# Performance work log

Hardware: AMD Instinct MI355X
Metric: run time of the kernel (lower is better)

Reference implementation:

```python
import jax, jax.numpy as jnp
import numpy as np

B, N, DIM = 2, 2048, 2048
H, KVH, HD = 16, 4, 128
N_REP = H // KVH
SCALE = np.float32(HD ** -0.5)


def setup_inputs() -> dict:
    key = jax.random.key(0)
    ks = jax.random.split(key, 5)
    x = jax.random.normal(ks[0], (B, N, DIM), dtype=jnp.float32)
    mask = jnp.tril(jnp.ones((N, N), dtype=jnp.int32))[None, None]  # [1,1,N,N] causal
    Wq = jax.random.normal(ks[1], (DIM, H * HD), dtype=jnp.float32) * (DIM ** -0.5)
    Wk = jax.random.normal(ks[2], (DIM, KVH * HD), dtype=jnp.float32) * (DIM ** -0.5)
    Wv = jax.random.normal(ks[3], (DIM, KVH * HD), dtype=jnp.float32) * (DIM ** -0.5)
    Wo = jax.random.normal(ks[4], (H * HD, DIM), dtype=jnp.float32) * ((H * HD) ** -0.5)
    return {"x": x, "mask": mask, "Wq": Wq, "Wk": Wk, "Wv": Wv, "Wo": Wo}


def reference(x, mask, Wq, Wk, Wv, Wo):
    Bx, Nx, _ = x.shape
    # projections -> [B, heads, N, head_dim]
    q = (x @ Wq).reshape(Bx, Nx, H, HD).transpose(0, 2, 1, 3)
    k = (x @ Wk).reshape(Bx, Nx, KVH, HD).transpose(0, 2, 1, 3)
    v = (x @ Wv).reshape(Bx, Nx, KVH, HD).transpose(0, 2, 1, 3)
    # repeat_interleave KV heads to match query heads (GQA)
    k = jnp.repeat(k, N_REP, axis=1)
    v = jnp.repeat(v, N_REP, axis=1)
    attn = jnp.einsum('bhqd,bhkd->bhqk', q, k) * SCALE
    attn = jnp.where(mask == 0, jnp.float32(-jnp.inf), attn)
    attn = jax.nn.softmax(attn, axis=-1)
    out = jnp.einsum('bhqk,bhkd->bhqd', attn, v)
    out = out.transpose(0, 2, 1, 3).reshape(Bx, Nx, H * HD)
    return out @ Wo
```

## Files before the change

### kernel.cpp

```cpp
#include <hip/hip_runtime.h>
#include <hip/hip_bf16.h>
#include <math.h>

typedef __bf16 bf16;
typedef bf16 bf16x8 __attribute__((ext_vector_type(8)));
typedef bf16 bf16x4v __attribute__((ext_vector_type(4)));
typedef float f32x4 __attribute__((ext_vector_type(4)));

#define GLD16(g, l) __builtin_amdgcn_global_load_lds(                          \
    (__attribute__((address_space(1))) void*)(g),                              \
    (__attribute__((address_space(3))) void*)(l), 16, 0, 0)

#define MFMA16(a, b, c) __builtin_amdgcn_mfma_f32_16x16x32_bf16((a), (b), (c), 0, 0, 0)

#if __has_builtin(__builtin_amdgcn_exp2f)
#define EXP2F(x) __builtin_amdgcn_exp2f(x)
#else
#define EXP2F(x) exp2f(x)
#endif

__device__ __forceinline__ f32x4 shfl_xor4(f32x4 a, int m) {
  f32x4 r;
  #pragma unroll
  for (int i = 0; i < 4; i++) r[i] = __shfl_xor(a[i], m);
  return r;
}

__global__ void cast_f32_bf16(const float* __restrict__ in, bf16* __restrict__ out, int n4) {
  int i = blockIdx.x * blockDim.x + threadIdx.x;
  if (i < n4) {
    float4 v = ((const float4*)in)[i];
    bf16x4v o;
    o.x = (bf16)v.x; o.y = (bf16)v.y; o.z = (bf16)v.z; o.w = (bf16)v.w;
    ((bf16x4v*)out)[i] = o;
  }
}

__global__ void transpose_cast(const float* __restrict__ in, bf16* __restrict__ out,
                               int colsIn, int outStride, int outRowOff, float scale) {
  __shared__ float t[32][33];
  int c0 = blockIdx.x * 32, r0 = blockIdx.y * 32;
  int tx = threadIdx.x, ty = threadIdx.y;
  #pragma unroll
  for (int i = 0; i < 32; i += 8)
    t[ty + i][tx] = in[(size_t)(r0 + ty + i) * colsIn + (c0 + tx)];
  __syncthreads();
  #pragma unroll
  for (int i = 0; i < 32; i += 8)
    out[(size_t)(outRowOff + c0 + ty + i) * outStride + (r0 + tx)] = (bf16)(t[tx][ty + i] * scale);
}

__global__ void transpose_v(const bf16* __restrict__ QKV, bf16* __restrict__ Vg) {
  __shared__ bf16 t[32][34];
  int n0 = blockIdx.x * 32, d0 = blockIdx.y * 32;
  int bk = blockIdx.z;
  int b = bk >> 2, kvh = bk & 3;
  const bf16* src = QKV + (size_t)b * 2048 * 3072 + 2560 + kvh * 128;
  bf16* dst = Vg + (size_t)bk * 128 * 2048;
  int tx = threadIdx.x, ty = threadIdx.y;
  #pragma unroll
  for (int i = 0; i < 32; i += 8)
    t[ty + i][tx] = src[(size_t)(n0 + ty + i) * 3072 + (d0 + tx)];
  __syncthreads();
  #pragma unroll
  for (int i = 0; i < 32; i += 8)
    dst[(size_t)(d0 + ty + i) * 2048 + (n0 + tx)] = t[tx][ty + i];
}

template <typename OutT>
__global__ __launch_bounds__(256, 2) void gemm_bt(const bf16* __restrict__ A,
                                                  const bf16* __restrict__ Bt,
                                                  OutT* __restrict__ C,
                                                  int M, int N, int K) {
  __shared__ __attribute__((aligned(16))) bf16 As[128 * 32];
  __shared__ __attribute__((aligned(16))) bf16 Bs[128 * 32];
  const int tid = threadIdx.x;
  const int lane = tid & 63;
  const int wave = tid >> 6;
  const int wm = wave >> 1, wn = wave & 1;
  const int l15 = lane & 15, quad = lane >> 4;
  const int rowBase = blockIdx.y * 128;
  const int colBase = blockIdx.x * 128;

  f32x4 acc[4][4] = {};

  const int cb0 = wave * 64;
  const int c0 = cb0 + lane;
  const int c1 = c0 + 256;
  const bf16* a0 = A + (size_t)(rowBase + (c0 >> 2)) * K + (c0 & 3) * 8;
  const bf16* a1 = A + (size_t)(rowBase + (c1 >> 2)) * K + (c1 & 3) * 8;
  const bf16* b0 = Bt + (size_t)(colBase + (c0 >> 2)) * K + (c0 & 3) * 8;
  const bf16* b1 = Bt + (size_t)(colBase + (c1 >> 2)) * K + (c1 & 3) * 8;
  bf16* lA0 = &As[cb0 * 8];
  bf16* lA1 = &As[(cb0 + 256) * 8];
  bf16* lB0 = &Bs[cb0 * 8];
  bf16* lB1 = &Bs[(cb0 + 256) * 8];

  for (int k0 = 0; k0 < K; k0 += 32) {
    GLD16(a0 + k0, lA0);
    GLD16(a1 + k0, lA1);
    GLD16(b0 + k0, lB0);
    GLD16(b1 + k0, lB1);
    __syncthreads();
    bf16x8 af[4], bfr[4];
    #pragma unroll
    for (int i = 0; i < 4; i++)
      af[i] = *(const bf16x8*)&As[(wm * 64 + i * 16 + l15) * 32 + quad * 8];
    #pragma unroll
    for (int i = 0; i < 4; i++)
      bfr[i] = *(const bf16x8*)&Bs[(wn * 64 + i * 16 + l15) * 32 + quad * 8];
    #pragma unroll
    for (int i = 0; i < 4; i++)
      #pragma unroll
      for (int j = 0; j < 4; j++)
        acc[i][j] = MFMA16(af[i], bfr[j], acc[i][j]);
    __syncthreads();
  }

  #pragma unroll
  for (int i = 0; i < 4; i++) {
    int row = rowBase + wm * 64 + i * 16 + quad * 4;
    #pragma unroll
    for (int j = 0; j < 4; j++) {
      int col = colBase + wn * 64 + j * 16 + l15;
      #pragma unroll
      for (int r = 0; r < 4; r++)
        C[(size_t)(row + r) * N + col] = (OutT)acc[i][j][r];
    }
  }
}

#define MASKV (-1e30f)

__device__ const unsigned char BMAP[22] = {
  28, 58, 24, 50, 20, 46, 36, 32,
  62, 59, 54, 51, 47, 42, 55, 63,
  0, 4, 8, 12, 16, 43
};

#define SLOT_F32 16640

__global__ __launch_bounds__(256, 2) void gqa_attn(const bf16* __restrict__ QKV,
                                                   const bf16* __restrict__ Vg,
                                                   bf16* __restrict__ Obf,
                                                   float* __restrict__ Part) {
  __shared__ __attribute__((aligned(16))) bf16 Kl[64 * 128];
  __shared__ __attribute__((aligned(16))) bf16 Vt[128 * 64];
  __shared__ __attribute__((aligned(16))) bf16 Pl[4][32 * 68];

  const int tid = threadIdx.x;
  const int lane = tid & 63;
  const int wave = tid >> 6;
  const int l15 = lane & 15, quad = lane >> 4;

  const int e = BMAP[blockIdx.x >> 5];
  const int bh = blockIdx.x & 31;
  const int qt = e >> 2;
  const int split = (e >> 1) & 1;
  const int half = e & 1;
  const int b = bh >> 4, h = bh & 15, kvh = h >> 2;
  const int q0 = qt * 128;
  const int nkt = 2 * qt + 2;
  const int kt_lo = (split && half) ? (nkt >> 1) : 0;
  const int kt_hi = (split && !half) ? (nkt >> 1) : nkt;

  const size_t rs = 3072;
  const bf16* Qb  = QKV + (size_t)b * 2048 * rs + h * 128;
  const bf16* Kb  = QKV + (size_t)b * 2048 * rs + 2048 + kvh * 128;
  const bf16* Vgb = Vg + (size_t)(b * 4 + kvh) * 128 * 2048;

  bf16x8 qf[2][4];
  #pragma unroll
  for (int mt = 0; mt < 2; mt++) {
    int row = q0 + wave * 32 + mt * 16 + l15;
    #pragma unroll
    for (int ks = 0; ks < 4; ks++)
      qf[mt][ks] = *(const bf16x8*)&Qb[(size_t)row * rs + ks * 32 + quad * 8];
  }

  bf16x8 ones8;
  #pragma unroll
  for (int i = 0; i < 8; i++) ones8[i] = (bf16)1.0f;

  const bf16* kp[4]; const bf16* vp[4];
  bf16* kl[4]; bf16* vl[4];
  #pragma unroll
  for (int t = 0; t < 4; t++) {
    int keyl = wave * 16 + t * 4 + (lane >> 4);
    int ck = (lane & 15) ^ (4 * (t & 1) + (lane >> 4));
    kp[t] = Kb + (size_t)(kt_lo * 64 + keyl) * rs + ck * 8;
    kl[t] = &Kl[(wave * 16 + t * 4) * 128];
    int dl = wave * 32 + t * 8 + (lane >> 3);
    int cv = (lane & 7) ^ (lane >> 3);
    vp[t] = Vgb + (size_t)dl * 2048 + kt_lo * 64 + cv * 8;
    vl[t] = &Vt[(wave * 32 + t * 8) * 64];
  }

  f32x4 oacc[2][8] = {};
  f32x4 lacc[2] = {};
  f32x4 mrow[2];
  #pragma unroll
  for (int mt = 0; mt < 2; mt++)
    #pragma unroll
    for (int r = 0; r < 4; r++) mrow[mt][r] = MASKV;

  const int myrow_hi = q0 + wave * 32 + 31;
  for (int kt = kt_lo; kt < kt_hi; kt++) {
    const int k0 = kt * 64;
    __syncthreads();
    #pragma unroll
    for (int t = 0; t < 4; t++) { GLD16(kp[t], kl[t]); kp[t] += 64 * rs; }
    #pragma unroll
    for (int t = 0; t < 4; t++) { GLD16(vp[t], vl[t]); vp[t] += 64; }
    __syncthreads();

    if (k0 > myrow_hi) continue;

    f32x4 s[2][4] = {};
    #pragma unroll
    for (int ks = 0; ks < 4; ks++) {
      #pragma unroll
      for (int nt = 0; nt < 4; nt++) {
        bf16x8 kf = *(const bf16x8*)&Kl[(nt * 16 + l15) * 128 +
                                        (((ks * 4 + quad) ^ (l15 & 7)) * 8)];
        s[0][nt] = MFMA16(qf[0][ks], kf, s[0][nt]);
        s[1][nt] = MFMA16(qf[1][ks], kf, s[1][nt]);
      }
    }
    if (kt >= nkt - 2) {
      #pragma unroll
      for (int mt = 0; mt < 2; mt++) {
        int rowb = q0 + wave * 32 + mt * 16 + quad * 4;
        #pragma unroll
        for (int nt = 0; nt < 4; nt++) {
          int col = k0 + nt * 16 + l15;
          #pragma unroll
          for (int r = 0; r < 4; r++)
            if (col > rowb + r) s[mt][nt][r] = MASKV;
        }
      }
    }
    #pragma unroll
    for (int mt = 0; mt < 2; mt++) {
      f32x4 mx = s[mt][0];
      #pragma unroll
      for (int nt = 1; nt < 4; nt++)
        #pragma unroll
        for (int r = 0; r < 4; r++) mx[r] = fmaxf(mx[r], s[mt][nt][r]);
      #pragma unroll
      for (int d = 1; d < 16; d <<= 1) {
        f32x4 o = shfl_xor4(mx, d);
        #pragma unroll
        for (int r = 0; r < 4; r++) mx[r] = fmaxf(mx[r], o[r]);
      }
      bool noresc = (mx[0] <= mrow[mt][0] + 8.f) && (mx[1] <= mrow[mt][1] + 8.f) &&
                    (mx[2] <= mrow[mt][2] + 8.f) && (mx[3] <= mrow[mt][3] + 8.f);
      if (!__all(noresc)) {
        f32x4 alpha;
        #pragma unroll
        for (int r = 0; r < 4; r++) {
          float mn = fmaxf(mrow[mt][r], mx[r]);
          alpha[r] = EXP2F(mrow[mt][r] - mn);
          mrow[mt][r] = mn;
        }
        #pragma unroll
        for (int no = 0; no < 8; no++)
          #pragma unroll
          for (int r = 0; r < 4; r++) oacc[mt][no][r] *= alpha[r];
        #pragma unroll
        for (int r = 0; r < 4; r++) lacc[mt][r] *= alpha[r];
      }
      #pragma unroll
      for (int nt = 0; nt < 4; nt++)
        #pragma unroll
        for (int r = 0; r < 4; r++) {
          float p = EXP2F(s[mt][nt][r] - mrow[mt][r]);
          Pl[wave][(mt * 16 + quad * 4 + r) * 68 + nt * 16 + l15] = (bf16)p;
        }
    }
    #pragma unroll
    for (int ks2 = 0; ks2 < 2; ks2++) {
      bf16x8 pf0 = *(const bf16x8*)&Pl[wave][l15 * 68 + ks2 * 32 + quad * 8];
      bf16x8 pf1 = *(const bf16x8*)&Pl[wave][(16 + l15) * 68 + ks2 * 32 + quad * 8];
      lacc[0] = MFMA16(pf0, ones8, lacc[0]);
      lacc[1] = MFMA16(pf1, ones8, lacc[1]);
      #pragma unroll
      for (int no = 0; no < 8; no++) {
        bf16x8 vf = *(const bf16x8*)&Vt[(no * 16 + l15) * 64 +
                                        (((ks2 * 4 + quad) ^ (l15 & 7)) * 8)];
        oacc[0][no] = MFMA16(pf0, vf, oacc[0][no]);
        oacc[1][no] = MFMA16(pf1, vf, oacc[1][no]);
      }
    }
  }

  if (!split) {
    #pragma unroll
    for (int mt = 0; mt < 2; mt++) {
      f32x4 linv;
      #pragma unroll
      for (int r = 0; r < 4; r++) linv[r] = 1.0f / lacc[mt][r];
      int row = q0 + wave * 32 + mt * 16 + quad * 4;
      #pragma unroll
      for (int no = 0; no < 8; no++) {
        int col = h * 128 + no * 16 + l15;
        #pragma unroll
        for (int r = 0; r < 4; r++)
          Obf[(size_t)(b * 2048 + row + r) * 2048 + col] = (bf16)(oacc[mt][no][r] * linv[r]);
      }
    }
  } else {
    const int fidx = bh * 6 + (qt - 10);
    float* slot = Part + (size_t)(fidx * 2 + half) * SLOT_F32;
    #pragma unroll
    for (int mt = 0; mt < 2; mt++) {
      int row = wave * 32 + mt * 16 + quad * 4;
      #pragma unroll
      for (int no = 0; no < 8; no++) {
        int col = no * 16 + l15;
        #pragma unroll
        for (int r = 0; r < 4; r++)
          slot[(row + r) * 128 + col] = oacc[mt][no][r];
      }
    }
    if (l15 == 0) {
      #pragma unroll
      for (int mt = 0; mt < 2; mt++)
        #pragma unroll
        for (int r = 0; r < 4; r++) {
          int row = wave * 32 + mt * 16 + quad * 4 + r;
          slot[16384 + row] = mrow[mt][r];
          slot[16512 + row] = lacc[mt][r];
        }
    }
  }
}

__global__ __launch_bounds__(256) void merge_split(const float* __restrict__ Part,
                                                   bf16* __restrict__ Obf) {
  const int fidx = blockIdx.x;
  const int bh = fidx / 6, qt = 10 + fidx % 6;
  const int b = bh >> 4, h = bh & 15;
  const int tid = threadIdx.x;
  const int cl = (tid & 31) * 4;
  const int r0 = tid >> 5;
  const float* s0 = Part + (size_t)(fidx * 2) * SLOT_F32;
  const float* s1 = s0 + SLOT_F32;
  #pragma unroll
  for (int i = 0; i < 16; i++) {
    int row = r0 + i * 8;
    float m0 = s0[16384 + row], l0 = s0[16512 + row];
    float m1 = s1[16384 + row], l1 = s1[16512 + row];
    float ms = fmaxf(m0, m1);
    float a0 = EXP2F(m0 - ms), a1 = EXP2F(m1 - ms);
    float linv = 1.0f / (l0 * a0 + l1 * a1);
    f32x4 v0 = *(const f32x4*)&s0[row * 128 + cl];
    f32x4 v1 = *(const f32x4*)&s1[row * 128 + cl];
    bf16x4v o;
    #pragma unroll
    for (int r = 0; r < 4; r++) o[r] = (bf16)((v0[r] * a0 + v1[r] * a1) * linv);
    *(bf16x4v*)&Obf[(size_t)(b * 2048 + qt * 128 + row) * 2048 + h * 128 + cl] = o;
  }
}

extern "C" void kernel_launch(void* const* d_in, const int* in_sizes, int n_in,
                              void* d_out, int out_size, void* d_ws, size_t ws_size,
                              hipStream_t stream) {
  const float* x  = (const float*)d_in[0];
  const float* Wq = (const float*)d_in[2];
  const float* Wk = (const float*)d_in[3];
  const float* Wv = (const float*)d_in[4];
  const float* Wo = (const float*)d_in[5];
  float* out = (float*)d_out;

  bf16* Xb    = (bf16*)d_ws;
  bf16* Wqkvt = Xb + 8388608;
  bf16* Wot   = Wqkvt + 6291456;
  bf16* QKV   = Wot + 4194304;
  bf16* Obf   = QKV + 12582912;
  bf16* Vg    = Obf + 8388608;

  float* Part = (float*)d_ws;

  const float qscale = (float)(0.08838834764831845 * 1.4426950408889634);

  cast_f32_bf16<<<8192, 256, 0, stream>>>(x, Xb, 2097152);
  dim3 tb(32, 8);
  transpose_cast<<<dim3(64, 64), tb, 0, stream>>>(Wq, Wqkvt, 2048, 2048, 0, qscale);
  transpose_cast<<<dim3(16, 64), tb, 0, stream>>>(Wk, Wqkvt, 512, 2048, 2048, 1.0f);
  transpose_cast<<<dim3(16, 64), tb, 0, stream>>>(Wv, Wqkvt, 512, 2048, 2560, 1.0f);
  transpose_cast<<<dim3(64, 64), tb, 0, stream>>>(Wo, Wot, 2048, 2048, 0, 1.0f);

  gemm_bt<bf16><<<dim3(24, 32), 256, 0, stream>>>(Xb, Wqkvt, QKV, 4096, 3072, 2048);
  transpose_v<<<dim3(64, 4, 8), tb, 0, stream>>>(QKV, Vg);
  gqa_attn<<<704, 256, 0, stream>>>(QKV, Vg, Obf, Part);
  merge_split<<<192, 256, 0, stream>>>(Part, Obf);
  gemm_bt<float><<<dim3(16, 32), 256, 0, stream>>>(Obf, Wot, out, 4096, 2048, 2048);
}
```

Before: 330.9 us.

## Merge prep kernels, fuse V transpose into QKV GEMM epilogue, persistent GEMM grid

The five cast and transpose launches become one prep kernel that dispatches on block index. The QKV GEMM now writes the V columns straight into the transposed Vg layout in its epilogue, which removes the separate transpose_v kernel. Both GEMMs switch to a 512-block grid-stride tile loop, cutting launch overhead and the extra V round-trip through memory. The trade-off is that V tiles are no longer written to QKV, and the transposed V stores are strided across rows and less coalesced.

```diff
diff --git a/kernel.cpp b/kernel.cpp
--- a/kernel.cpp
+++ b/kernel.cpp
@@ -26,52 +26,48 @@
   return r;
 }
 
-__global__ void cast_f32_bf16(const float* __restrict__ in, bf16* __restrict__ out, int n4) {
-  int i = blockIdx.x * blockDim.x + threadIdx.x;
-  if (i < n4) {
-    float4 v = ((const float4*)in)[i];
+__global__ __launch_bounds__(256) void prep(const float* __restrict__ x,
+                                            const float* __restrict__ Wq,
+                                            const float* __restrict__ Wk,
+                                            const float* __restrict__ Wv,
+                                            const float* __restrict__ Wo,
+                                            bf16* __restrict__ Xb,
+                                            bf16* __restrict__ Wqkvt,
+                                            bf16* __restrict__ Wot,
+                                            float qscale) {
+  const int id = blockIdx.x;
+  const int tid = threadIdx.x;
+  if (id >= 10240) {
+    int i = (id - 10240) * 256 + tid;
+    float4 v = ((const float4*)x)[i];
     bf16x4v o;
     o.x = (bf16)v.x; o.y = (bf16)v.y; o.z = (bf16)v.z; o.w = (bf16)v.w;
-    ((bf16x4v*)out)[i] = o;
-  }
-}
-
-__global__ void transpose_cast(const float* __restrict__ in, bf16* __restrict__ out,
-                               int colsIn, int outStride, int outRowOff, float scale) {
+    ((bf16x4v*)Xb)[i] = o;
+    return;
+  }
   __shared__ float t[32][33];
-  int c0 = blockIdx.x * 32, r0 = blockIdx.y * 32;
-  int tx = threadIdx.x, ty = threadIdx.y;
+  const float* in; bf16* out; int colsIn, outRowOff, bx, by; float scale;
+  if (id < 4096)      { in = Wq; out = Wqkvt; colsIn = 2048; outRowOff = 0;    scale = qscale; bx = id & 63;          by = id >> 6; }
+  else if (id < 5120) { in = Wk; out = Wqkvt; colsIn = 512;  outRowOff = 2048; scale = 1.0f;   bx = (id - 4096) & 15; by = (id - 4096) >> 4; }
+  else if (id < 6144) { in = Wv; out = Wqkvt; colsIn = 512;  outRowOff = 2560; scale = 1.0f;   bx = (id - 5120) & 15; by = (id - 5120) >> 4; }
+  else                { in = Wo; out = Wot;   colsIn = 2048; outRowOff = 0;    scale = 1.0f;   bx = (id - 6144) & 63; by = (id - 6144) >> 6; }
+  const int c0 = bx * 32, r0 = by * 32;
+  const int tx = tid & 31, ty = tid >> 5;
   #pragma unroll
   for (int i = 0; i < 32; i += 8)
     t[ty + i][tx] = in[(size_t)(r0 + ty + i) * colsIn + (c0 + tx)];
   __syncthreads();
   #pragma unroll
   for (int i = 0; i < 32; i += 8)
-    out[(size_t)(outRowOff + c0 + ty + i) * outStride + (r0 + tx)] = (bf16)(t[tx][ty + i] * scale);
-}
-
-__global__ void transpose_v(const bf16* __restrict__ QKV, bf16* __restrict__ Vg) {
-  __shared__ bf16 t[32][34];
-  int n0 = blockIdx.x * 32, d0 = blockIdx.y * 32;
-  int bk = blockIdx.z;
-  int b = bk >> 2, kvh = bk & 3;
-  const bf16* src = QKV + (size_t)b * 2048 * 3072 + 2560 + kvh * 128;
-  bf16* dst = Vg + (size_t)bk * 128 * 2048;
-  int tx = threadIdx.x, ty = threadIdx.y;
-  #pragma unroll
-  for (int i = 0; i < 32; i += 8)
-    t[ty + i][tx] = src[(size_t)(n0 + ty + i) * 3072 + (d0 + tx)];
-  __syncthreads();
-  #pragma unroll
-  for (int i = 0; i < 32; i += 8)
-    dst[(size_t)(d0 + ty + i) * 2048 + (n0 + tx)] = t[tx][ty + i];
+    out[(size_t)(outRowOff + c0 + ty + i) * 2048 + (r0 + tx)] = (bf16)(t[tx][ty + i] * scale);
 }
 
 template <typename OutT>
 __global__ __launch_bounds__(256, 2) void gemm_bt(const bf16* __restrict__ A,
                                                   const bf16* __restrict__ Bt,
                                                   OutT* __restrict__ C,
-                                                  int M, int N, int K) {
+                                                  bf16* __restrict__ Vg,
+                                                  int N, int K, int numTiles) {
   __shared__ __attribute__((aligned(16))) bf16 As[128 * 32];
   __shared__ __attribute__((aligned(16))) bf16 Bs[128 * 32];
   const int tid = threadIdx.x;
@@ -79,53 +75,74 @@
   const int wave = tid >> 6;
   const int wm = wave >> 1, wn = wave & 1;
   const int l15 = lane & 15, quad = lane >> 4;
-  const int rowBase = blockIdx.y * 128;
-  const int colBase = blockIdx.x * 128;
-
-  f32x4 acc[4][4] = {};
+  const int nCol = N >> 7;
 
   const int cb0 = wave * 64;
   const int c0 = cb0 + lane;
   const int c1 = c0 + 256;
-  const bf16* a0 = A + (size_t)(rowBase + (c0 >> 2)) * K + (c0 & 3) * 8;
-  const bf16* a1 = A + (size_t)(rowBase + (c1 >> 2)) * K + (c1 & 3) * 8;
-  const bf16* b0 = Bt + (size_t)(colBase + (c0 >> 2)) * K + (c0 & 3) * 8;
-  const bf16* b1 = Bt + (size_t)(colBase + (c1 >> 2)) * K + (c1 & 3) * 8;
   bf16* lA0 = &As[cb0 * 8];
   bf16* lA1 = &As[(cb0 + 256) * 8];
   bf16* lB0 = &Bs[cb0 * 8];
   bf16* lB1 = &Bs[(cb0 + 256) * 8];
 
-  for (int k0 = 0; k0 < K; k0 += 32) {
-    GLD16(a0 + k0, lA0);
-    GLD16(a1 + k0, lA1);
-    GLD16(b0 + k0, lB0);
-    GLD16(b1 + k0, lB1);
-    __syncthreads();
-    bf16x8 af[4], bfr[4];
-    #pragma unroll
-    for (int i = 0; i < 4; i++)
-      af[i] = *(const bf16x8*)&As[(wm * 64 + i * 16 + l15) * 32 + quad * 8];
-    #pragma unroll
-    for (int i = 0; i < 4; i++)
-      bfr[i] = *(const bf16x8*)&Bs[(wn * 64 + i * 16 + l15) * 32 + quad * 8];
-    #pragma unroll
-    for (int i = 0; i < 4; i++)
-      #pragma unroll
-      for (int j = 0; j < 4; j++)
-        acc[i][j] = MFMA16(af[i], bfr[j], acc[i][j]);
-    __syncthreads();
-  }
-
-  #pragma unroll
-  for (int i = 0; i < 4; i++) {
-    int row = rowBase + wm * 64 + i * 16 + quad * 4;
-    #pragma unroll
-    for (int j = 0; j < 4; j++) {
-      int col = colBase + wn * 64 + j * 16 + l15;
-      #pragma unroll
-      for (int r = 0; r < 4; r++)
-        C[(size_t)(row + r) * N + col] = (OutT)acc[i][j][r];
+  for (int t = blockIdx.x; t < numTiles; t += 512) {
+    const int rowBase = (t / nCol) * 128;
+    const int colBase = (t % nCol) * 128;
+    const bf16* a0 = A + (size_t)(rowBase + (c0 >> 2)) * K + (c0 & 3) * 8;
+    const bf16* a1 = A + (size_t)(rowBase + (c1 >> 2)) * K + (c1 & 3) * 8;
+    const bf16* b0 = Bt + (size_t)(colBase + (c0 >> 2)) * K + (c0 & 3) * 8;
+    const bf16* b1 = Bt + (size_t)(colBase + (c1 >> 2)) * K + (c1 & 3) * 8;
+
+    f32x4 acc[4][4] = {};
+    for (int k0 = 0; k0 < K; k0 += 32) {
+      GLD16(a0 + k0, lA0);
+      GLD16(a1 + k0, lA1);
+      GLD16(b0 + k0, lB0);
+      GLD16(b1 + k0, lB1);
+      __syncthreads();
+      bf16x8 af[4], bfr[4];
+      #pragma unroll
+      for (int i = 0; i < 4; i++)
+        af[i] = *(const bf16x8*)&As[(wm * 64 + i * 16 + l15) * 32 + quad * 8];
+      #pragma unroll
+      for (int i = 0; i < 4; i++)
+        bfr[i] = *(const bf16x8*)&Bs[(wn * 64 + i * 16 + l15) * 32 + quad * 8];
+      #pragma unroll
+      for (int i = 0; i < 4; i++)
+        #pragma unroll
+        for (int j = 0; j < 4; j++)
+          acc[i][j] = MFMA16(af[i], bfr[j], acc[i][j]);
+      __syncthreads();
+    }
+
+    if (Vg != nullptr && colBase >= 2560) {
+      const int kvh = (colBase - 2560) >> 7;
+      #pragma unroll
+      for (int i = 0; i < 4; i++) {
+        int row = rowBase + wm * 64 + i * 16 + quad * 4;
+        int bb = row >> 11;
+        int n0 = row & 2047;
+        #pragma unroll
+        for (int j = 0; j < 4; j++) {
+          int d = wn * 64 + j * 16 + l15;
+          bf16x4v o;
+          #pragma unroll
+          for (int r = 0; r < 4; r++) o[r] = (bf16)acc[i][j][r];
+          *(bf16x4v*)&Vg[((size_t)(bb * 4 + kvh) * 128 + d) * 2048 + n0] = o;
+        }
+      }
+    } else {
+      #pragma unroll
+      for (int i = 0; i < 4; i++) {
+        int row = rowBase + wm * 64 + i * 16 + quad * 4;
+        #pragma unroll
+        for (int j = 0; j < 4; j++) {
+          int col = colBase + wn * 64 + j * 16 + l15;
+          #pragma unroll
+          for (int r = 0; r < 4; r++)
+            C[(size_t)(row + r) * N + col] = (OutT)acc[i][j][r];
+        }
+      }
     }
   }
 }
@@ -384,16 +401,9 @@
 
   const float qscale = (float)(0.08838834764831845 * 1.4426950408889634);
 
-  cast_f32_bf16<<<8192, 256, 0, stream>>>(x, Xb, 2097152);
-  dim3 tb(32, 8);
-  transpose_cast<<<dim3(64, 64), tb, 0, stream>>>(Wq, Wqkvt, 2048, 2048, 0, qscale);
-  transpose_cast<<<dim3(16, 64), tb, 0, stream>>>(Wk, Wqkvt, 512, 2048, 2048, 1.0f);
-  transpose_cast<<<dim3(16, 64), tb, 0, stream>>>(Wv, Wqkvt, 512, 2048, 2560, 1.0f);
-  transpose_cast<<<dim3(64, 64), tb, 0, stream>>>(Wo, Wot, 2048, 2048, 0, 1.0f);
-
-  gemm_bt<bf16><<<dim3(24, 32), 256, 0, stream>>>(Xb, Wqkvt, QKV, 4096, 3072, 2048);
-  transpose_v<<<dim3(64, 4, 8), tb, 0, stream>>>(QKV, Vg);
+  prep<<<18432, 256, 0, stream>>>(x, Wq, Wk, Wv, Wo, Xb, Wqkvt, Wot, qscale);
+  gemm_bt<bf16><<<512, 256, 0, stream>>>(Xb, Wqkvt, QKV, Vg, 3072, 2048, 768);
   gqa_attn<<<704, 256, 0, stream>>>(QKV, Vg, Obf, Part);
   merge_split<<<192, 256, 0, stream>>>(Part, Obf);
-  gemm_bt<float><<<dim3(16, 32), 256, 0, stream>>>(Obf, Wot, out, 4096, 2048, 2048);
-}
+  gemm_bt<float><<<512, 256, 0, stream>>>(Obf, Wot, out, (bf16*)nullptr, 2048, 2048, 512);
+}
```

New measurement: 342.6 us. +3.5%, slower.
